# Optimization experiments

Hardware: AMD Instinct MI355X
Metric: run time of the kernel (lower is better)

The kernel has to match this reference:

```python
import jax, jax.numpy as jnp
import numpy as np

EMB_DIM = 256
DICT_SIZE = 8192
EPSILON = 1e-05


def setup_inputs() -> dict:
    key = jax.random.key(0)
    k_x, k_e = jax.random.split(key)
    x = jax.random.normal(k_x, (32, EMB_DIM, 32, 32), dtype=jnp.float32)
    embed = jax.random.normal(k_e, (DICT_SIZE, EMB_DIM), dtype=jnp.float32)
    embed = embed / jnp.linalg.norm(embed, axis=1, keepdims=True)  # F.normalize p=2
    track_num = jnp.zeros((DICT_SIZE, 1), dtype=jnp.float32)
    track_enc = embed  # buffers initialized as embed.clone()
    return {"x": x, "embed": embed, "track_num": track_num, "track_enc": track_enc}


def reference(x, embed, track_num, track_enc):
    b, c, h, w = x.shape
    K = embed.shape[0]
    # flatten: transpose(1,-1) -> [b,w,h,c], reshape -> [N, c]
    flat = jnp.transpose(x, (0, 3, 2, 1)).reshape(-1, c)  # [N, D]

    # KNN (k=1, l2): squared distance is monotone in l2, argmin identical
    x2 = jnp.sum(flat * flat, axis=1, keepdims=True)          # [N,1]
    e2 = jnp.sum(embed * embed, axis=1)                        # [K]
    d2 = x2 - 2.0 * (flat @ embed.T) + e2[None, :]             # [N,K]
    ids = jnp.argmin(d2, axis=1)                               # [N] int

    vqs_flat = embed[ids]                                      # [N, D]

    # EMA update, first-time path: buffers copied from raw statistics
    counts = jax.ops.segment_sum(jnp.ones_like(flat[:, 0]), ids, num_segments=K)
    new_track_num = counts[:, None]                            # [K,1]
    new_track_enc = jax.ops.segment_sum(flat, ids, num_segments=K)  # onehot.T @ flatten
    factor = 1.0 + EPSILON * K / new_track_num.sum()
    new_embed = new_track_enc * factor / (new_track_num + EPSILON)

    # restore spatial layout: view(b,w,h,c).transpose(1,-1) -> [b,c,h,w]
    vqs = jnp.transpose(vqs_flat.reshape(b, w, h, c), (0, 3, 2, 1))
    ids_out = jnp.transpose(ids.reshape(b, w, h), (0, 2, 1))   # [b,h,w]

    st_out = x + jax.lax.stop_gradient(vqs - x)                # straight-through
    loss = jnp.mean((jax.lax.stop_gradient(vqs) - x) ** 2)     # mse(vqs.detach(), input)
    return st_out, loss, ids_out, new_embed, new_track_num, new_track_enc
```

## Files before the change

### kernel.cpp

```cpp
#include <hip/hip_runtime.h>

#define NR 32768
#define CD 256
#define KD 8192

typedef __attribute__((ext_vector_type(8))) _Float16 f16x8;
typedef __attribute__((ext_vector_type(4))) _Float16 f16x4;
typedef __attribute__((ext_vector_type(4))) float f32x4;

#define F_XH      0ull
#define F_XL      4194304ull
#define F_EH      8388608ull
#define F_EMBT    9437184ull
#define F_E2N     11534336ull
#define F_E2NP    11542528ull
#define F_IDS     11550720ull
#define F_FLAGCNT 11583488ull
#define F_LOSS    11583489ull
#define F_FLAGLST 11583490ull
#define F_COUNTS  11616258ull
#define F_CURSOR  11624450ull
#define F_OFFS    11632642ull
#define F_BUCKET  11640834ull
#define F_PBD     11673602ull
#define F_PBI     11689986ull

#define OUT_ST   0ull
#define OUT_LOSS 8388608ull
#define OUT_IDS  8388609ull
#define OUT_NEMB 8421377ull
#define OUT_NUM  10518529ull
#define OUT_ENC  10526721ull

__device__ __forceinline__ float np_pw128(const float* p) {
    float r0 = p[0], r1 = p[1], r2 = p[2], r3 = p[3];
    float r4 = p[4], r5 = p[5], r6 = p[6], r7 = p[7];
    for (int i = 8; i < 128; i += 8) {
        r0 += p[i + 0]; r1 += p[i + 1]; r2 += p[i + 2]; r3 += p[i + 3];
        r4 += p[i + 4]; r5 += p[i + 5]; r6 += p[i + 6]; r7 += p[i + 7];
    }
    return ((r0 + r1) + (r2 + r3)) + ((r4 + r5) + (r6 + r7));
}

__global__ void k_cvt_x(const float* __restrict__ x,
                        _Float16* __restrict__ xh, _Float16* __restrict__ xl) {
    __shared__ float t[32 * 529];
    const int bx = blockIdx.x;
    const int b = bx >> 4, cg = (bx >> 1) & 7, h0 = (bx & 1) * 16;
    const int tid = threadIdx.x;
    const float* src = x + ((size_t)(b * 256 + cg * 32)) * 1024 + h0 * 32;
    for (int i = 0; i < 64; ++i) {
        int e = i * 256 + tid;
        int c = e >> 9, rem = e & 511;
        int hh = rem >> 5, w = rem & 31;
        t[c * 529 + hh * 33 + w] = src[(size_t)c * 1024 + hh * 32 + w];
    }
    __syncthreads();
    const int ni = tid >> 5, c = tid & 31;
    for (int i = 0; i < 64; ++i) {
        int ns = i * 8 + ni;
        int w = ns >> 4, hh = ns & 15;
        float v = t[c * 529 + hh * 33 + w];
        _Float16 hi = (_Float16)v;
        _Float16 lo = (_Float16)(v - (float)hi);
        size_t o = ((size_t)(b * 1024 + w * 32 + h0 + hh)) * 256 + cg * 32 + c;
        xh[o] = hi; xl[o] = lo;
    }
}

__global__ void k_prep_e(const float* __restrict__ embed,
                         _Float16* __restrict__ eh, float* __restrict__ e2n) {
    int wave = threadIdx.x >> 6, lane = threadIdx.x & 63;
    int k = blockIdx.x * 4 + wave;
    float4 v = *(const float4*)(embed + (size_t)k * CD + lane * 4);
    f16x4 h;
    h[0] = (_Float16)v.x; h[1] = (_Float16)v.y;
    h[2] = (_Float16)v.z; h[3] = (_Float16)v.w;
    *(f16x4*)&eh[(size_t)k * CD + lane * 4] = h;
    float s = v.x * v.x + v.y * v.y + v.z * v.z + v.w * v.w;
    #pragma unroll
    for (int off = 1; off < 64; off <<= 1) s += __shfl_xor(s, off);
    if (lane == 0) e2n[k] = -0.5f * s;
}

__global__ void k_e2np(const float* __restrict__ embed, float* __restrict__ e2np) {
    const int lane = threadIdx.x & 63;
    const int wv = threadIdx.x >> 6;
    const int k = blockIdx.x * 32 + wv * 8 + (lane >> 3);
    const int j = lane & 7;
    float hsum[2];
    #pragma unroll
    for (int half = 0; half < 2; ++half) {
        float r = 0.f;
        for (int i = 0; i < 16; ++i) {
            float v = embed[(size_t)k * CD + half * 128 + j + i * 8];
            float sq = v * v;
            asm volatile("" : "+v"(sq));
            r += sq;
        }
        float s = r + __shfl_xor(r, 1);
        s = s + __shfl_xor(s, 2);
        s = s + __shfl_xor(s, 4);
        hsum[half] = s;
    }
    if (j == 0) e2np[k] = hsum[0] + hsum[1];
}

__global__ void k_epose(const float* __restrict__ embed, float* __restrict__ embedT) {
    int kt = blockIdx.x >> 2, ct = blockIdx.x & 3;
    __shared__ float t[64][65];
    int tid = threadIdx.x;
    #pragma unroll
    for (int i = 0; i < 16; ++i) {
        int e = tid + i * 256; int r = e >> 6, c = e & 63;
        t[r][c] = embed[(size_t)(kt * 64 + r) * CD + ct * 64 + c];
    }
    __syncthreads();
    #pragma unroll
    for (int i = 0; i < 16; ++i) {
        int e = tid + i * 256; int c = e >> 6, r = e & 63;
        embedT[(size_t)(ct * 64 + c) * KD + kt * 64 + r] = t[r][c];
    }
}

#define LDSB_OFF 81920
#define LDSM_OFF 147456

#define STAGE_STEP(SBO, ADVN)                                                     \
    do {                                                                          \
        __builtin_amdgcn_global_load_lds(                                         \
            (const __attribute__((address_space(1))) unsigned int*)(bs0),         \
            (__attribute__((address_space(3))) unsigned int*)(smem + (SBO) + tid * 16), \
            16, 0, 0);                                                            \
        __builtin_amdgcn_global_load_lds(                                         \
            (const __attribute__((address_space(1))) unsigned int*)(bs1),         \
            (__attribute__((address_space(3))) unsigned int*)(smem + (SBO) + 8192 + tid * 16), \
            16, 0, 0);                                                            \
        bs0 += (ADVN); bs1 += (ADVN);                                             \
    } while (0)

#define PIPE_BAR()                                                                \
    do {                                                                          \
        __builtin_amdgcn_sched_barrier(0);                                        \
        asm volatile("s_waitcnt vmcnt(2)" ::: "memory");                          \
        __builtin_amdgcn_s_barrier();                                             \
        __builtin_amdgcn_sched_barrier(0);                                        \
    } while (0)

__global__ __launch_bounds__(512, 1) void k_mfma(
    const _Float16* __restrict__ xh, const _Float16* __restrict__ eh,
    const float* __restrict__ e2n, int* __restrict__ ids,
    int* __restrict__ flag_cnt, int* __restrict__ flag_list,
    int* __restrict__ counts)
{
    __shared__ __attribute__((aligned(16))) char smem[153600];
    const int tid = threadIdx.x;
    const int w = tid >> 6, l = tid & 63;
    const int wm = w & 3, wn = w >> 2;
    const int lr = l & 15, q = l >> 4;
    const int n0 = blockIdx.x * 128;

    #pragma unroll
    for (int i = 0; i < 8; ++i) {
        const int row = i * 16 + (tid >> 5);
        const int slot = tid & 31;
        const _Float16* src = xh + (size_t)(n0 + row) * 256 + ((slot ^ (row & 15)) * 8);
        __builtin_amdgcn_global_load_lds(
            (const __attribute__((address_space(1))) unsigned int*)src,
            (__attribute__((address_space(3))) unsigned int*)
                (smem + LDSB_OFF + row * 512 + slot * 16),
            16, 0, 0);
    }

    const int code0 = tid >> 2;
    const int code1 = 128 + code0;
    const int slot4 = tid & 3;
    const _Float16* bs0 = eh + (size_t)code0 * 256 + ((slot4 ^ ((code0 >> 1) & 3)) * 8);
    const _Float16* bs1 = eh + (size_t)code1 * 256 + ((slot4 ^ ((code1 >> 1) & 3)) * 8);

    STAGE_STEP(0, 32);
    STAGE_STEP(16384, 32);
    STAGE_STEP(32768, 32);

    f32x4 e2c[4];
    #pragma unroll
    for (int m = 0; m < 4; ++m)
        e2c[m] = *(const f32x4*)(e2n + wm * 64 + m * 16 + q * 4);

    PIPE_BAR();

    f32x4 acc[4][4];
    float m1[4], m2[4]; int i1[4];
    #pragma unroll
    for (int n = 0; n < 4; ++n) { m1[n] = -3.4e38f; m2[n] = -3.4e38f; i1[n] = 0; }

    int faoff[4];
    #pragma unroll
    for (int m = 0; m < 4; ++m) {
        const int code = wm * 64 + m * 16 + lr;
        faoff[m] = code * 64 + ((q ^ ((code >> 1) & 3)) * 16);
    }
    int vb[4];
    #pragma unroll
    for (int n = 0; n < 4; ++n) {
        const int row = wn * 64 + n * 16 + lr;
        vb[n] = LDSB_OFF + row * 512 + ((q ^ (lr & 3)) * 16) + ((lr >> 2) * 64);
    }

    auto COMP = [&](int cc, int cbOff, bool cinit) {
        f16x8 fa[4], fb[4];
        #pragma unroll
        for (int m = 0; m < 4; ++m)
            fa[m] = *(const f16x8*)(smem + cbOff + faoff[m]);
        #pragma unroll
        for (int n = 0; n < 4; ++n)
            fb[n] = *(const f16x8*)(smem + (vb[n] ^ (cc << 6)));
        if (cinit) {
            #pragma unroll
            for (int m = 0; m < 4; ++m)
                #pragma unroll
                for (int n = 0; n < 4; ++n)
                    acc[m][n] = __builtin_amdgcn_mfma_f32_16x16x32_f16(fa[m], fb[n], e2c[m], 0, 0, 0);
        } else {
            #pragma unroll
            for (int m = 0; m < 4; ++m)
                #pragma unroll
                for (int n = 0; n < 4; ++n)
                    acc[m][n] = __builtin_amdgcn_mfma_f32_16x16x32_f16(fa[m], fb[n], acc[m][n], 0, 0, 0);
        }
    };

    auto FOLD = [&](int cg) {
        const int kb = cg * 256 + wm * 64 + q * 4;
        #pragma unroll
        for (int n = 0; n < 4; ++n)
            #pragma unroll
            for (int m = 0; m < 4; ++m)
                #pragma unroll
                for (int r = 0; r < 4; ++r) {
                    const float v = acc[m][n][r];
                    const bool g = v > m1[n];
                    m2[n] = fmaxf(m2[n], fminf(v, m1[n]));
                    m1[n] = fmaxf(m1[n], v);
                    i1[n] = g ? (kb + m * 16 + r) : i1[n];
                }
    };

    int cbo0 = 0, cbo1 = 16384, sbo0 = 49152, sbo1 = 65536;
    #define ADV(x) do { (x) += 32768; if ((x) >= 81920) (x) -= 81920; } while (0)

    #pragma unroll 1
    for (int cg = 0; cg < 32; ++cg) {
        STAGE_STEP(sbo0, 32);
        STAGE_STEP(sbo1, 32);
        COMP(0, cbo0, true);
        COMP(1, cbo1, false);
        PIPE_BAR();
        ADV(cbo0); ADV(cbo1); ADV(sbo0); ADV(sbo1);

        STAGE_STEP(sbo0, 32);
        STAGE_STEP(sbo1, 32);
        COMP(2, cbo0, false);
        COMP(3, cbo1, false);
        PIPE_BAR();
        ADV(cbo0); ADV(cbo1); ADV(sbo0); ADV(sbo1);

        STAGE_STEP(sbo0, 65312);
        STAGE_STEP(sbo1, 32);
        if (cg < 31) {
            #pragma unroll
            for (int m = 0; m < 4; ++m)
                e2c[m] = *(const f32x4*)(e2n + (cg + 1) * 256 + wm * 64 + m * 16 + q * 4);
        }
        COMP(4, cbo0, false);
        COMP(5, cbo1, false);
        PIPE_BAR();
        ADV(cbo0); ADV(cbo1); ADV(sbo0); ADV(sbo1);

        STAGE_STEP(sbo0, 32);
        STAGE_STEP(sbo1, 32);
        COMP(6, cbo0, false);
        COMP(7, cbo1, false);
        FOLD(cg);
        PIPE_BAR();
        ADV(cbo0); ADV(cbo1); ADV(sbo0); ADV(sbo1);
    }
    #undef ADV

    #pragma unroll
    for (int off = 16; off < 64; off <<= 1) {
        #pragma unroll
        for (int n = 0; n < 4; ++n) {
            const float om1 = __shfl_xor(m1[n], off);
            const float om2 = __shfl_xor(m2[n], off);
            const int   oi  = __shfl_xor(i1[n], off);
            const bool g = om1 > m1[n];
            m2[n] = fmaxf(fminf(m1[n], om1), fmaxf(m2[n], om2));
            m1[n] = fmaxf(m1[n], om1);
            i1[n] = g ? oi : i1[n];
        }
    }
    float* sm1 = (float*)(smem + LDSM_OFF);
    float* sm2 = (float*)(smem + LDSM_OFF + 2048);
    int*   si1 = (int*)  (smem + LDSM_OFF + 4096);
    __syncthreads();
    if (q == 0) {
        #pragma unroll
        for (int n = 0; n < 4; ++n) {
            const int row = wn * 64 + n * 16 + lr;
            sm1[wm * 128 + row] = m1[n];
            sm2[wm * 128 + row] = m2[n];
            si1[wm * 128 + row] = i1[n];
        }
    }
    __syncthreads();
    if (tid < 128) {
        float a1 = sm1[tid], a2 = sm2[tid]; int ai = si1[tid];
        #pragma unroll
        for (int wq = 1; wq < 4; ++wq) {
            const float b1 = sm1[wq * 128 + tid], b2 = sm2[wq * 128 + tid];
            const int bi = si1[wq * 128 + tid];
            const bool g = b1 > a1;
            a2 = fmaxf(fminf(a1, b1), fmaxf(a2, b2));
            a1 = fmaxf(a1, b1);
            ai = g ? bi : ai;
        }
        const int n = n0 + tid;
        ids[n] = ai;
        atomicAdd(&counts[ai], 1);
        if (a1 - a2 < 2.5e-3f) {
            int p = atomicAdd(flag_cnt, 1);
            flag_list[p] = n;
        }
    }
}

#define RG 16
__global__ __launch_bounds__(256) void k_rescore(
    const float* __restrict__ x, const float* __restrict__ embedT,
    const float* __restrict__ e2np, const int* __restrict__ flag_cnt,
    const int* __restrict__ flag_list, float* __restrict__ pbd, int* __restrict__ pbi)
{
    __shared__ float rowl[RG][256];
    __shared__ float sq[RG][256];
    __shared__ float x2s[RG];
    __shared__ float bdA[256];
    __shared__ int   biA[256];
    const int tid = threadIdx.x;
    int cnt = *flag_cnt; if (cnt > 2048) cnt = 2048;
    const int ngroups = (cnt + RG - 1) / RG;
    const int kt = blockIdx.x & 7;
    for (int g = blockIdx.x >> 3; g < ngroups; g += 64) {
        #pragma unroll
        for (int i = 0; i < RG; ++i) {
            int f = g * RG + i;
            float v = 0.f;
            if (f < cnt) {
                int n = flag_list[f];
                int b = n >> 10, wq = (n >> 5) & 31, hq = n & 31;
                v = x[((size_t)(b * 256 + tid)) * 1024 + hq * 32 + wq];
            }
            rowl[i][tid] = v;
            sq[i][tid] = v * v;
        }
        __syncthreads();
        if (tid < RG) x2s[tid] = np_pw128(sq[tid]) + np_pw128(sq[tid] + 128);
        __syncthreads();

        float acc[RG][4];
        #pragma unroll
        for (int r = 0; r < RG; ++r)
            #pragma unroll
            for (int e = 0; e < 4; ++e) acc[r][e] = 0.f;
        for (int c = 0; c < 256; ++c) {
            const f32x4 bv = *(const f32x4*)&embedT[(size_t)c * KD + kt * 1024 + tid * 4];
            #pragma unroll
            for (int r = 0; r < RG; ++r) {
                const float av = rowl[r][c];
                acc[r][0] = fmaf(av, bv[0], acc[r][0]);
                acc[r][1] = fmaf(av, bv[1], acc[r][1]);
                acc[r][2] = fmaf(av, bv[2], acc[r][2]);
                acc[r][3] = fmaf(av, bv[3], acc[r][3]);
            }
        }
        #pragma unroll
        for (int r = 0; r < RG; ++r) {
            float bd = 3.4e38f; int bi = 0x7fffffff;
            #pragma unroll
            for (int e = 0; e < 4; ++e) {
                const int k = kt * 1024 + tid * 4 + e;
                const float d2 = (x2s[r] - 2.0f * acc[r][e]) + e2np[k];
                if (d2 < bd || (d2 == bd && k < bi)) { bd = d2; bi = k; }
            }
            bdA[tid] = bd; biA[tid] = bi;
            __syncthreads();
            for (int off = 128; off > 0; off >>= 1) {
                if (tid < off) {
                    float od = bdA[tid + off]; int oi = biA[tid + off];
                    if (od < bdA[tid] || (od == bdA[tid] && oi < biA[tid])) {
                        bdA[tid] = od; biA[tid] = oi;
                    }
                }
                __syncthreads();
            }
            if (tid == 0) {
                int f = g * RG + r;
                if (f < cnt) { pbd[f * 8 + kt] = bdA[0]; pbi[f * 8 + kt] = biA[0]; }
            }
            __syncthreads();
        }
    }
}

__global__ void k_flagmerge(const int* __restrict__ flag_cnt, const int* __restrict__ flag_list,
                            const float* __restrict__ pbd, const int* __restrict__ pbi,
                            int* __restrict__ ids, int* __restrict__ counts) {
    int cnt = *flag_cnt; if (cnt > 2048) cnt = 2048;
    int f = blockIdx.x * 256 + threadIdx.x;
    if (f >= cnt) return;
    float bd = pbd[f * 8]; int bi = pbi[f * 8];
    #pragma unroll
    for (int kt = 1; kt < 8; ++kt) {
        float d = pbd[f * 8 + kt]; int i = pbi[f * 8 + kt];
        if (d < bd || (d == bd && i < bi)) { bd = d; bi = i; }
    }
    const int n = flag_list[f];
    const int old = ids[n];
    if (bi != old) {
        ids[n] = bi;
        atomicAdd(&counts[old], -1);
        atomicAdd(&counts[bi], 1);
    }
}

__global__ __launch_bounds__(256) void k_output(
    const float* __restrict__ x, const float* __restrict__ embed,
    const int* __restrict__ ids, float* __restrict__ st,
    float* __restrict__ loss_ws)
{
    const int b = blockIdx.x >> 5, h = blockIdx.x & 31;
    const int tid = threadIdx.x;
    __shared__ int sid[32];
    __shared__ float vq[256 * 33];
    if (tid < 32) sid[tid] = ids[b * 1024 + tid * 32 + h];
    __syncthreads();
    #pragma unroll 4
    for (int w = 0; w < 32; ++w) {
        vq[tid * 33 + w] = embed[(size_t)sid[w] * CD + tid];
    }
    __syncthreads();
    float lsum = 0.f;
    const size_t base0 = (((size_t)b * 256) * 32 + h) * 32;
    #pragma unroll 8
    for (int it = 0; it < 32; ++it) {
        const int c = it * 8 + (tid >> 5);
        const int w = tid & 31;
        const size_t a = base0 + (size_t)c * 1024 + w;
        const float v = vq[c * 33 + w];
        const float xv = x[a];
        st[a] = v;
        const float d = v - xv;
        lsum = fmaf(d, d, lsum);
    }
    #pragma unroll
    for (int off = 1; off < 64; off <<= 1) lsum += __shfl_xor(lsum, off);
    if ((tid & 63) == 0) atomicAdd(loss_ws, lsum);
}

__global__ void k_ids(const int* __restrict__ ids, float* __restrict__ ids_out) {
    int e = blockIdx.x * 256 + threadIdx.x;
    int b = e >> 10, h = (e >> 5) & 31, w = e & 31;
    ids_out[e] = (float)ids[b * 1024 + w * 32 + h];
}

__global__ void k_scan(const int* __restrict__ counts, int* __restrict__ offs,
                       float* __restrict__ track_num) {
    __shared__ int ps[257];
    const int tid = threadIdx.x;
    int loc[32]; int s = 0;
    const int base = tid * 32;
    #pragma unroll
    for (int j = 0; j < 32; ++j) { loc[j] = s; s += counts[base + j]; }
    ps[tid + 1] = s;
    if (tid == 0) ps[0] = 0;
    __syncthreads();
    if (tid == 0) for (int i = 1; i <= 256; ++i) ps[i] += ps[i - 1];
    __syncthreads();
    const int pre = ps[tid];
    #pragma unroll
    for (int j = 0; j < 32; ++j) {
        offs[base + j] = pre + loc[j];
        track_num[base + j] = (float)counts[base + j];
    }
}

__global__ void k_fill(const int* __restrict__ ids, const int* __restrict__ offs,
                       int* __restrict__ cursor, int* __restrict__ bucket) {
    int n = blockIdx.x * 256 + threadIdx.x;
    int id = ids[n];
    int p = atomicAdd(&cursor[id], 1);
    bucket[offs[id] + p] = n;
}

__global__ void k_gather(const _Float16* __restrict__ xh, const _Float16* __restrict__ xl,
                         const int* __restrict__ offs, const int* __restrict__ counts,
                         const int* __restrict__ bucket, float* __restrict__ enc) {
    const int k = blockIdx.x, c = threadIdx.x;
    const int o = offs[k], cnt = counts[k];
    float s = 0.f;
    for (int i = 0; i < cnt; ++i) {
        int n = bucket[o + i];
        s += (float)xh[(size_t)n * CD + c] + (float)xl[(size_t)n * CD + c];
    }
    enc[(size_t)k * CD + c] = s;
}

__global__ void k_final(const float* __restrict__ track_num, const float* __restrict__ track_enc,
                        float* __restrict__ new_embed, const float* __restrict__ loss_ws,
                        float* __restrict__ loss_out)
{
    const size_t e = (size_t)blockIdx.x * 256 + threadIdx.x;
    const int k = (int)(e >> 8);
    const float factor = 1.0f + (1e-5f * 8192.0f) / 32768.0f;
    new_embed[e] = track_enc[e] * factor / (track_num[k] + 1e-5f);
    if (e == 0) loss_out[0] = loss_ws[0] * (1.0f / 8388608.0f);
}

extern "C" void kernel_launch(void* const* d_in, const int* in_sizes, int n_in,
                              void* d_out, int out_size, void* d_ws, size_t ws_size,
                              hipStream_t stream)
{
    const float* x     = (const float*)d_in[0];
    const float* embed = (const float*)d_in[1];
    float* out = (float*)d_out;
    float* ws  = (float*)d_ws;

    _Float16* xh = (_Float16*)(ws + F_XH);
    _Float16* xl = (_Float16*)(ws + F_XL);
    _Float16* eh = (_Float16*)(ws + F_EH);
    float* embedT    = ws + F_EMBT;
    float* e2n       = ws + F_E2N;
    float* e2np      = ws + F_E2NP;
    int*   ids       = (int*)(ws + F_IDS);
    int*   flag_cnt  = (int*)(ws + F_FLAGCNT);
    float* loss_ws   = ws + F_LOSS;
    int*   flag_list = (int*)(ws + F_FLAGLST);
    int*   counts    = (int*)(ws + F_COUNTS);
    int*   cursor    = (int*)(ws + F_CURSOR);
    int*   offs      = (int*)(ws + F_OFFS);
    int*   bucket    = (int*)(ws + F_BUCKET);
    float* pbd       = ws + F_PBD;
    int*   pbi       = (int*)(ws + F_PBI);

    hipMemsetAsync(ws + F_FLAGCNT, 0, 2 * sizeof(float), stream);
    hipMemsetAsync(ws + F_COUNTS, 0, 2 * 8192 * sizeof(float), stream);

    k_cvt_x    <<<512,  256, 0, stream>>>(x, xh, xl);
    k_prep_e   <<<2048, 256, 0, stream>>>(embed, eh, e2n);
    k_e2np     <<<256,  256, 0, stream>>>(embed, e2np);
    k_epose    <<<512,  256, 0, stream>>>(embed, embedT);
    k_mfma     <<<256,  512, 0, stream>>>(xh, eh, e2n, ids, flag_cnt, flag_list, counts);
    k_rescore  <<<512,  256, 0, stream>>>(x, embedT, e2np, flag_cnt, flag_list, pbd, pbi);
    k_flagmerge<<<8,    256, 0, stream>>>(flag_cnt, flag_list, pbd, pbi, ids, counts);
    k_output   <<<1024, 256, 0, stream>>>(x, embed, ids, out + OUT_ST, loss_ws);
    k_ids      <<<128,  256, 0, stream>>>(ids, out + OUT_IDS);
    k_scan     <<<1,    256, 0, stream>>>(counts, offs, out + OUT_NUM);
    k_fill     <<<128,  256, 0, stream>>>(ids, offs, cursor, bucket);
    k_gather   <<<8192, 256, 0, stream>>>(xh, xl, offs, counts, bucket, out + OUT_ENC);
    k_final    <<<8192, 256, 0, stream>>>(out + OUT_NUM, out + OUT_ENC, out + OUT_NEMB,
                                          loss_ws, out + OUT_LOSS);
}
```

Baseline: 378.0 us.

## Enlarge codebook tile to 512 codes per group with triple-buffered LDS staging

Each wave now computes an 8x4 MFMA tile (128 codes by 64 rows) instead of 4x4, and the block processes 512 codes per group over 16 iterations instead of 256 over 32. Each B-fragment load from LDS is therefore reused across twice as many codes. The pipeline becomes a three-slot ring of 32 KB stages with four global-to-LDS loads per interval, and the e2 bias is added during the fold instead of being used as the MFMA initial accumulator. MFMA sections are wrapped in s_setprio. The cost is doubled accumulator registers and a larger LDS footprint, which adds register pressure and a risk of spills.

```diff
diff --git a/kernel.cpp b/kernel.cpp
--- a/kernel.cpp
+++ b/kernel.cpp
@@ -123,28 +123,79 @@
     }
 }
 
-#define LDSB_OFF 81920
-#define LDSM_OFF 147456
-
-#define STAGE_STEP(SBO, ADVN)                                                     \
-    do {                                                                          \
-        __builtin_amdgcn_global_load_lds(                                         \
-            (const __attribute__((address_space(1))) unsigned int*)(bs0),         \
-            (__attribute__((address_space(3))) unsigned int*)(smem + (SBO) + tid * 16), \
-            16, 0, 0);                                                            \
-        __builtin_amdgcn_global_load_lds(                                         \
-            (const __attribute__((address_space(1))) unsigned int*)(bs1),         \
-            (__attribute__((address_space(3))) unsigned int*)(smem + (SBO) + 8192 + tid * 16), \
-            16, 0, 0);                                                            \
-        bs0 += (ADVN); bs1 += (ADVN);                                             \
-    } while (0)
+#define LDSB_OFF 98304
+#define LDSM_OFF 32768
+
+#define GLD16(PTR, DST)                                                           \
+    __builtin_amdgcn_global_load_lds(                                             \
+        (const __attribute__((address_space(1))) unsigned int*)(PTR),             \
+        (__attribute__((address_space(3))) unsigned int*)(DST), 16, 0, 0)
 
 #define PIPE_BAR()                                                                \
     do {                                                                          \
         __builtin_amdgcn_sched_barrier(0);                                        \
-        asm volatile("s_waitcnt vmcnt(2)" ::: "memory");                          \
+        asm volatile("s_waitcnt vmcnt(4)" ::: "memory");                          \
         __builtin_amdgcn_s_barrier();                                             \
         __builtin_amdgcn_sched_barrier(0);                                        \
+    } while (0)
+
+#define ADVR(x) do { (x) += 32768; if ((x) >= 98304) (x) -= 98304; } while (0)
+
+#define INTERVAL(P, ADVB, DO_E2C, DO_FOLD)                                        \
+    do {                                                                          \
+        if (DO_E2C) {                                                             \
+            const float* e2b = e2n + cg * 512 + wm * 128 + q * 4;                 \
+            _Pragma("unroll")                                                     \
+            for (int m = 0; m < 8; ++m) e2c[m] = *(const f32x4*)(e2b + m * 16);   \
+        }                                                                         \
+        GLD16(bs0, smem + sbo + tid * 16);                                        \
+        GLD16(bs1, smem + sbo + 8192 + tid * 16);                                 \
+        GLD16(bs2, smem + sbo + 16384 + tid * 16);                                \
+        GLD16(bs3, smem + sbo + 24576 + tid * 16);                                \
+        bs0 += (ADVB); bs1 += (ADVB); bs2 += (ADVB); bs3 += (ADVB);               \
+        {                                                                         \
+            f16x8 fa[8], fb[4];                                                   \
+            _Pragma("unroll")                                                     \
+            for (int m = 0; m < 8; ++m)                                           \
+                fa[m] = *(const f16x8*)(smem + cbo + faoff[m]);                   \
+            _Pragma("unroll")                                                     \
+            for (int n = 0; n < 4; ++n)                                           \
+                fb[n] = *(const f16x8*)(smem + (vb[n] ^ ((P) << 6)));             \
+            __builtin_amdgcn_s_setprio(1);                                        \
+            if ((P) == 0) {                                                       \
+                _Pragma("unroll")                                                 \
+                for (int m = 0; m < 8; ++m)                                       \
+                    _Pragma("unroll")                                             \
+                    for (int n = 0; n < 4; ++n)                                   \
+                        acc[m][n] = __builtin_amdgcn_mfma_f32_16x16x32_f16(       \
+                            fa[m], fb[n], zinit, 0, 0, 0);                        \
+            } else {                                                              \
+                _Pragma("unroll")                                                 \
+                for (int m = 0; m < 8; ++m)                                       \
+                    _Pragma("unroll")                                             \
+                    for (int n = 0; n < 4; ++n)                                   \
+                        acc[m][n] = __builtin_amdgcn_mfma_f32_16x16x32_f16(       \
+                            fa[m], fb[n], acc[m][n], 0, 0, 0);                    \
+            }                                                                     \
+            __builtin_amdgcn_s_setprio(0);                                        \
+        }                                                                         \
+        if (DO_FOLD) {                                                            \
+            const int kb = cg * 512 + wm * 128 + q * 4;                           \
+            _Pragma("unroll")                                                     \
+            for (int n = 0; n < 4; ++n)                                           \
+                _Pragma("unroll")                                                 \
+                for (int m = 0; m < 8; ++m)                                       \
+                    _Pragma("unroll")                                             \
+                    for (int r = 0; r < 4; ++r) {                                 \
+                        const float v = acc[m][n][r] + e2c[m][r];                 \
+                        const bool g = v > m1[n];                                 \
+                        m2[n] = fmaxf(m2[n], fminf(v, m1[n]));                    \
+                        m1[n] = fmaxf(m1[n], v);                                  \
+                        i1[n] = g ? (kb + m * 16 + r) : i1[n];                    \
+                    }                                                             \
+        }                                                                         \
+        PIPE_BAR();                                                               \
+        ADVR(cbo); ADVR(sbo);                                                     \
     } while (0)
 
 __global__ __launch_bounds__(512, 1) void k_mfma(
@@ -153,7 +204,7 @@
     int* __restrict__ flag_cnt, int* __restrict__ flag_list,
     int* __restrict__ counts)
 {
-    __shared__ __attribute__((aligned(16))) char smem[153600];
+    __shared__ __attribute__((aligned(16))) char smem[163840];
     const int tid = threadIdx.x;
     const int w = tid >> 6, l = tid & 63;
     const int wm = w & 3, wn = w >> 2;
@@ -165,40 +216,41 @@
         const int row = i * 16 + (tid >> 5);
         const int slot = tid & 31;
         const _Float16* src = xh + (size_t)(n0 + row) * 256 + ((slot ^ (row & 15)) * 8);
-        __builtin_amdgcn_global_load_lds(
-            (const __attribute__((address_space(1))) unsigned int*)src,
-            (__attribute__((address_space(3))) unsigned int*)
-                (smem + LDSB_OFF + row * 512 + slot * 16),
-            16, 0, 0);
-    }
-
-    const int code0 = tid >> 2;
-    const int code1 = 128 + code0;
-    const int slot4 = tid & 3;
-    const _Float16* bs0 = eh + (size_t)code0 * 256 + ((slot4 ^ ((code0 >> 1) & 3)) * 8);
-    const _Float16* bs1 = eh + (size_t)code1 * 256 + ((slot4 ^ ((code1 >> 1) & 3)) * 8);
-
-    STAGE_STEP(0, 32);
-    STAGE_STEP(16384, 32);
-    STAGE_STEP(32768, 32);
-
-    f32x4 e2c[4];
-    #pragma unroll
-    for (int m = 0; m < 4; ++m)
-        e2c[m] = *(const f32x4*)(e2n + wm * 64 + m * 16 + q * 4);
+        GLD16(src, smem + LDSB_OFF + row * 512 + slot * 16);
+    }
+
+    const int codeb = tid >> 2;
+    const int sw = ((tid & 3) ^ ((codeb >> 1) & 3)) * 8;
+    const _Float16* bs0 = eh + (size_t)(codeb +   0) * 256 + sw;
+    const _Float16* bs1 = eh + (size_t)(codeb + 128) * 256 + sw;
+    const _Float16* bs2 = eh + (size_t)(codeb + 256) * 256 + sw;
+    const _Float16* bs3 = eh + (size_t)(codeb + 384) * 256 + sw;
+
+    GLD16(bs0, smem + 0     + tid * 16);
+    GLD16(bs1, smem + 8192  + tid * 16);
+    GLD16(bs2, smem + 16384 + tid * 16);
+    GLD16(bs3, smem + 24576 + tid * 16);
+    bs0 += 32; bs1 += 32; bs2 += 32; bs3 += 32;
+    GLD16(bs0, smem + 32768 + tid * 16);
+    GLD16(bs1, smem + 40960 + tid * 16);
+    GLD16(bs2, smem + 49152 + tid * 16);
+    GLD16(bs3, smem + 57344 + tid * 16);
+    bs0 += 32; bs1 += 32; bs2 += 32; bs3 += 32;
 
     PIPE_BAR();
 
-    f32x4 acc[4][4];
+    f32x4 acc[8][4];
+    f32x4 e2c[8];
+    const f32x4 zinit = {0.f, 0.f, 0.f, 0.f};
     float m1[4], m2[4]; int i1[4];
     #pragma unroll
     for (int n = 0; n < 4; ++n) { m1[n] = -3.4e38f; m2[n] = -3.4e38f; i1[n] = 0; }
 
-    int faoff[4];
-    #pragma unroll
-    for (int m = 0; m < 4; ++m) {
-        const int code = wm * 64 + m * 16 + lr;
-        faoff[m] = code * 64 + ((q ^ ((code >> 1) & 3)) * 16);
+    int faoff[8];
+    #pragma unroll
+    for (int m = 0; m < 8; ++m) {
+        const int code = wm * 128 + m * 16 + lr;
+        faoff[m] = code * 64 + ((q ^ ((lr >> 1) & 3)) * 16);
     }
     int vb[4];
     #pragma unroll
@@ -207,85 +259,18 @@
         vb[n] = LDSB_OFF + row * 512 + ((q ^ (lr & 3)) * 16) + ((lr >> 2) * 64);
     }
 
-    auto COMP = [&](int cc, int cbOff, bool cinit) {
-        f16x8 fa[4], fb[4];
-        #pragma unroll
-        for (int m = 0; m < 4; ++m)
-            fa[m] = *(const f16x8*)(smem + cbOff + faoff[m]);
-        #pragma unroll
-        for (int n = 0; n < 4; ++n)
-            fb[n] = *(const f16x8*)(smem + (vb[n] ^ (cc << 6)));
-        if (cinit) {
-            #pragma unroll
-            for (int m = 0; m < 4; ++m)
-                #pragma unroll
-                for (int n = 0; n < 4; ++n)
-                    acc[m][n] = __builtin_amdgcn_mfma_f32_16x16x32_f16(fa[m], fb[n], e2c[m], 0, 0, 0);
-        } else {
-            #pragma unroll
-            for (int m = 0; m < 4; ++m)
-                #pragma unroll
-                for (int n = 0; n < 4; ++n)
-                    acc[m][n] = __builtin_amdgcn_mfma_f32_16x16x32_f16(fa[m], fb[n], acc[m][n], 0, 0, 0);
-        }
-    };
-
-    auto FOLD = [&](int cg) {
-        const int kb = cg * 256 + wm * 64 + q * 4;
-        #pragma unroll
-        for (int n = 0; n < 4; ++n)
-            #pragma unroll
-            for (int m = 0; m < 4; ++m)
-                #pragma unroll
-                for (int r = 0; r < 4; ++r) {
-                    const float v = acc[m][n][r];
-                    const bool g = v > m1[n];
-                    m2[n] = fmaxf(m2[n], fminf(v, m1[n]));
-                    m1[n] = fmaxf(m1[n], v);
-                    i1[n] = g ? (kb + m * 16 + r) : i1[n];
-                }
-    };
-
-    int cbo0 = 0, cbo1 = 16384, sbo0 = 49152, sbo1 = 65536;
-    #define ADV(x) do { (x) += 32768; if ((x) >= 81920) (x) -= 81920; } while (0)
-
+    int cbo = 0, sbo = 65536;
     #pragma unroll 1
-    for (int cg = 0; cg < 32; ++cg) {
-        STAGE_STEP(sbo0, 32);
-        STAGE_STEP(sbo1, 32);
-        COMP(0, cbo0, true);
-        COMP(1, cbo1, false);
-        PIPE_BAR();
-        ADV(cbo0); ADV(cbo1); ADV(sbo0); ADV(sbo1);
-
-        STAGE_STEP(sbo0, 32);
-        STAGE_STEP(sbo1, 32);
-        COMP(2, cbo0, false);
-        COMP(3, cbo1, false);
-        PIPE_BAR();
-        ADV(cbo0); ADV(cbo1); ADV(sbo0); ADV(sbo1);
-
-        STAGE_STEP(sbo0, 65312);
-        STAGE_STEP(sbo1, 32);
-        if (cg < 31) {
-            #pragma unroll
-            for (int m = 0; m < 4; ++m)
-                e2c[m] = *(const f32x4*)(e2n + (cg + 1) * 256 + wm * 64 + m * 16 + q * 4);
-        }
-        COMP(4, cbo0, false);
-        COMP(5, cbo1, false);
-        PIPE_BAR();
-        ADV(cbo0); ADV(cbo1); ADV(sbo0); ADV(sbo1);
-
-        STAGE_STEP(sbo0, 32);
-        STAGE_STEP(sbo1, 32);
-        COMP(6, cbo0, false);
-        COMP(7, cbo1, false);
-        FOLD(cg);
-        PIPE_BAR();
-        ADV(cbo0); ADV(cbo1); ADV(sbo0); ADV(sbo1);
-    }
-    #undef ADV
+    for (int cg = 0; cg < 16; ++cg) {
+        INTERVAL(0, 32,     false, false);
+        INTERVAL(1, 32,     false, false);
+        INTERVAL(2, 32,     false, false);
+        INTERVAL(3, 32,     false, false);
+        INTERVAL(4, 32,     false, false);
+        INTERVAL(5, 130848, false, false);
+        INTERVAL(6, 32,     true,  false);
+        INTERVAL(7, 32,     false, true);
+    }
 
     #pragma unroll
     for (int off = 16; off < 64; off <<= 1) {
```

Result: slower. 390.3 us (+3.3%).
